# Performance work log

Hardware: AMD Instinct MI355X
Metric: run time of the kernel (lower is better)

Reference implementation:

```python
import jax, jax.numpy as jnp
import numpy as np

B, T, D, H = 2, 2048, 1024, 16
DH = D // H
THETA = 10000.0
MAX_SEQ_LEN = 2048


def setup_inputs() -> dict:
    key = jax.random.key(0)
    kx, kqkv, ko = jax.random.split(key, 3)
    # trunc_normal init matching the torch Linear (std=sqrt(2/(fan_in+fan_out)), clipped at 3 sigma)
    sigma_qkv = (2.0 / (D + 3 * D)) ** 0.5
    sigma_o = (2.0 / (D + D)) ** 0.5
    W_qkv = jax.random.truncated_normal(kqkv, -3.0, 3.0, (3 * D, D), jnp.float32) * sigma_qkv
    W_o = jax.random.truncated_normal(ko, -3.0, 3.0, (D, D), jnp.float32) * sigma_o
    # RoPE caches: angles[t, i] = t / theta^(2i/d_k)
    dims = jnp.arange(0, DH, 2, dtype=jnp.float32)
    inv_freq = 1.0 / (THETA ** (dims / DH))  # [DH/2]
    angles = jnp.arange(MAX_SEQ_LEN, dtype=jnp.float32)[:, None] * inv_freq[None, :]  # [T, DH/2]
    return {
        "x": jax.random.normal(kx, (B, T, D), jnp.float32),
        "token_positions": jnp.arange(T, dtype=jnp.int64 if jax.config.jax_enable_x64 else jnp.int32),
        "W_qkv": W_qkv,
        "W_o": W_o,
        "cos_cached": jnp.cos(angles),
        "sin_cached": jnp.sin(angles),
    }


def _apply_rope(x, cos, sin):
    # x: [b, h, t, dh]; cos/sin: [t, dh/2] broadcast over (b, h)
    x1 = x[..., 0::2]
    x2 = x[..., 1::2]
    r1 = x1 * cos - x2 * sin
    r2 = x1 * sin + x2 * cos
    # interleave back: (.., dh/2, 2) -> (.., dh)
    return jnp.stack([r1, r2], axis=-1).reshape(x.shape)


def reference(x, token_positions, W_qkv, W_o, cos_cached, sin_cached):
    b, t, d = x.shape
    qkv = jnp.einsum("btd,ed->bte", x, W_qkv)  # [b, t, 3d]
    q, k, v = jnp.split(qkv, 3, axis=-1)

    def to_heads(z):
        return z.reshape(b, t, H, DH).transpose(0, 2, 1, 3)  # [b, h, t, dh]

    q, k, v = to_heads(q), to_heads(k), to_heads(v)

    cos = cos_cached[token_positions]  # [t, dh/2]
    sin = sin_cached[token_positions]
    q = _apply_rope(q, cos, sin)
    k = _apply_rope(k, cos, sin)

    scale = 1.0 / jnp.sqrt(jnp.asarray(DH, x.dtype))
    scores = jnp.einsum("bhqd,bhkd->bhqk", q, k) * scale  # full TxT (naive, matches source)
    causal = jnp.tril(jnp.ones((t, t), dtype=bool))  # [t, t]
    scores = jnp.where(causal[None, None, :, :], scores, -jnp.inf)
    attn = jax.nn.softmax(scores, axis=-1)
    out = jnp.einsum("bhqk,bhkd->bhqd", attn, v)  # [b, h, t, dh]
    out = out.transpose(0, 2, 1, 3).reshape(b, t, d)
    return jnp.einsum("btd,ed->bte", out, W_o)
```

## Files before the change

### kernel.cpp

```cpp
#include <hip/hip_runtime.h>
#include <hip/hip_bf16.h>
#include <stdint.h>

#define Bn  2
#define Tn  2048
#define Dn  1024
#define Hn  16
#define DHn 64
#define QSCALE 0.1803368801111204f

typedef unsigned short u16;
typedef __attribute__((ext_vector_type(8))) short s16x8;
typedef __attribute__((ext_vector_type(8))) unsigned short u16x8;
typedef __attribute__((ext_vector_type(4))) unsigned short u16x4;
typedef __attribute__((ext_vector_type(4))) float f32x4;

#define MFMA(a, b, c) __builtin_amdgcn_mfma_f32_16x16x32_bf16((a), (b), (c), 0, 0, 0)

__device__ __forceinline__ u16 f2bf(float f) {
  union { __hip_bfloat16 b; u16 u; } c;
  c.b = __float2bfloat16(f);
  return c.u;
}
__device__ __forceinline__ float bf2f(u16 u) {
  union { u16 u; __hip_bfloat16 b; } c;
  c.u = u;
  return __bfloat162float(c.b);
}

__device__ __forceinline__ void lds16(void* lds, const void* g) {
  __builtin_amdgcn_global_load_lds((__attribute__((address_space(1))) void*)(g),
                                   (__attribute__((address_space(3))) void*)(lds), 16, 0, 0);
}

__global__ __launch_bounds__(256) void k_cvt3(
    const float* __restrict__ s0, int n0,
    const float* __restrict__ s1, int n1,
    const float* __restrict__ s2, int n2,
    u16* __restrict__ d01, u16* __restrict__ d2) {
  int i = blockIdx.x * blockDim.x + threadIdx.x;
  const int stride = gridDim.x * blockDim.x;
  const int nt = n0 + n1 + n2;
  for (; i < nt; i += stride) {
    float4 v;
    u16x4 o;
    if (i < n0 + n1) {
      v = (i < n0) ? ((const float4*)s0)[i] : ((const float4*)s1)[i - n0];
      o[0] = f2bf(v.x); o[1] = f2bf(v.y); o[2] = f2bf(v.z); o[3] = f2bf(v.w);
      ((u16x4*)d01)[i] = o;
    } else {
      v = ((const float4*)s2)[i - n0 - n1];
      o[0] = f2bf(v.x); o[1] = f2bf(v.y); o[2] = f2bf(v.z); o[3] = f2bf(v.w);
      ((u16x4*)d2)[i - n0 - n1] = o;
    }
  }
}

__global__ __launch_bounds__(256) void k_qkv(
    const u16* __restrict__ xb, const u16* __restrict__ wb,
    const int* __restrict__ tokpos,
    const float* __restrict__ cosc, const float* __restrict__ sinc,
    u16* __restrict__ qb, u16* __restrict__ kb, u16* __restrict__ vtb)
{
  __shared__ u16 smem[17408];
  const int tid  = threadIdx.x;
  const int bcol = blockIdx.x;
  const int brow = blockIdx.y;
  const int lane = tid & 63, w = tid >> 6;
  const int wr = w >> 1, wc = w & 1;
  const int l15 = lane & 15, l4 = lane >> 4;
  const int lrow = lane >> 2;
  const int gsw  = (((lane & 3) ^ ((lrow >> 1) & 3)) * 8);
  const int rsw  = (l15 >> 1) & 3;

  const u16* xrow = xb + (size_t)(brow * 128) * 1024;
  const u16* wrow = wb + (size_t)(bcol * 128) * 1024;

  f32x4 acc[4][4] = {};

  {
    const int r0 = w * 32;
    lds16(&smem[r0 * 32],              xrow + (size_t)(r0 + lrow) * 1024 + gsw);
    lds16(&smem[(r0 + 16) * 32],       xrow + (size_t)(r0 + 16 + lrow) * 1024 + gsw);
    lds16(&smem[8192 + r0 * 32],       wrow + (size_t)(r0 + lrow) * 1024 + gsw);
    lds16(&smem[8192 + (r0 + 16) * 32],wrow + (size_t)(r0 + 16 + lrow) * 1024 + gsw);
  }

  for (int kt = 0; kt < 32; ++kt) {
    const int cur = kt & 1;
    const u16* Asb = smem + cur * 4096;
    const u16* Bsb = smem + 8192 + cur * 4096;
    if (kt < 31) {
      u16* Asn = smem + (cur ^ 1) * 4096;
      u16* Bsn = smem + 8192 + (cur ^ 1) * 4096;
      const int k1 = (kt + 1) * 32;
      const int r0 = w * 32;
      lds16(&Asn[r0 * 32],        xrow + (size_t)(r0 + lrow) * 1024 + k1 + gsw);
      lds16(&Asn[(r0 + 16) * 32], xrow + (size_t)(r0 + 16 + lrow) * 1024 + k1 + gsw);
      lds16(&Bsn[r0 * 32],        wrow + (size_t)(r0 + lrow) * 1024 + k1 + gsw);
      lds16(&Bsn[(r0 + 16) * 32], wrow + (size_t)(r0 + 16 + lrow) * 1024 + k1 + gsw);
      asm volatile("s_waitcnt vmcnt(4)" ::: "memory");
    } else {
      asm volatile("s_waitcnt vmcnt(0)" ::: "memory");
    }
    __builtin_amdgcn_s_barrier();
    __builtin_amdgcn_sched_barrier(0);
    __builtin_amdgcn_s_setprio(1);
    {
      const int gr = (l4 ^ rsw) * 8;
      s16x8 af[4], bf[4];
#pragma unroll
      for (int m = 0; m < 4; ++m)
        af[m] = *(const s16x8*)&Asb[(wr * 64 + m * 16 + l15) * 32 + gr];
#pragma unroll
      for (int n = 0; n < 4; ++n)
        bf[n] = *(const s16x8*)&Bsb[(wc * 64 + n * 16 + l15) * 32 + gr];
#pragma unroll
      for (int m = 0; m < 4; ++m)
#pragma unroll
        for (int n = 0; n < 4; ++n)
          acc[m][n] = MFMA(af[m], bf[n], acc[m][n]);
    }
    __builtin_amdgcn_s_setprio(0);
    __builtin_amdgcn_sched_barrier(0);
    __builtin_amdgcn_s_barrier();
  }

#pragma unroll
  for (int m = 0; m < 4; ++m)
#pragma unroll
    for (int n = 0; n < 4; ++n)
#pragma unroll
      for (int r = 0; r < 4; ++r)
        smem[(wr * 64 + m * 16 + l4 * 4 + r) * 136 + wc * 64 + n * 16 + l15] =
            f2bf(acc[m][n][r]);
  __syncthreads();

  if (bcol < 16) {
    u16* dst; float sc;
    if (bcol < 8) { dst = qb; sc = QSCALE; } else { dst = kb; sc = 1.0f; }
#pragma unroll
    for (int ph = 0; ph < 8; ++ph) {
      const int task = ph * 256 + tid;
      const int lr   = task >> 4;
      const int cg   = task & 15;
      const int rowg = brow * 128 + lr;
      const int b = rowg >> 11, t = rowg & 2047;
      const int rem = (bcol * 128 + cg * 8) & 1023;
      const int h = rem >> 6, dh0 = rem & 63;
      u16x8 v = *(const u16x8*)&smem[lr * 136 + cg * 8];
      const int pos = tokpos[t];
      const float4 cv = *(const float4*)&cosc[pos * 32 + (dh0 >> 1)];
      const float4 sv = *(const float4*)&sinc[pos * 32 + (dh0 >> 1)];
      const float cc[4] = {cv.x, cv.y, cv.z, cv.w};
      const float ss[4] = {sv.x, sv.y, sv.z, sv.w};
      u16x8 o;
#pragma unroll
      for (int p = 0; p < 4; ++p) {
        const float x1 = bf2f(v[2 * p]), x2 = bf2f(v[2 * p + 1]);
        o[2 * p]     = f2bf((x1 * cc[p] - x2 * ss[p]) * sc);
        o[2 * p + 1] = f2bf((x1 * ss[p] + x2 * cc[p]) * sc);
      }
      *(u16x8*)(dst + ((size_t)(b * Hn + h) * Tn + t) * DHn + dh0) = o;
    }
  } else {
    const int b  = (brow * 128) >> 11;
    const int t0 = (brow * 128) & 2047;
#pragma unroll
    for (int ph = 0; ph < 8; ++ph) {
      const int task = ph * 256 + tid;
      const int col = task & 127;
      const int tg  = task >> 7;
      const int h  = 2 * (bcol - 16) + (col >> 6);
      const int dh = col & 63;
      u16x8 v;
#pragma unroll
      for (int j = 0; j < 8; ++j) v[j] = smem[(tg * 8 + j) * 136 + col];
      *(u16x8*)(vtb + ((size_t)(b * Hn + h) * DHn + dh) * Tn + t0 + tg * 8) = v;
    }
  }
}

__global__ __launch_bounds__(512) void k_attn(
    const u16* __restrict__ qbuf, const u16* __restrict__ kbuf,
    const u16* __restrict__ vtb, u16* __restrict__ ob)
{
  __shared__ u16 Ks[2][128][64];
  __shared__ u16 Vs[64][128];
  __shared__ u16 Ps[2][8][16][64];

  const int tid  = threadIdx.x;
  const int lane = tid & 63, w = tid >> 6;
  const int l15 = lane & 15, l4 = lane >> 4;
  const int rsw  = l15 & 7;
  const int kgsw = ((lane & 7) ^ (lane >> 3)) * 8;

  const int lin = blockIdx.x;
  const int bh  = lin & 31;
  const int a   = (lin >> 5) & 7, rb = lin >> 8;
  const int qblk = rb ? (15 - a) : a;
  const int b = bh >> 4, h = bh & 15;

  const u16* Qh = qbuf + (size_t)bh * Tn * DHn;
  const u16* Kh = kbuf + (size_t)bh * Tn * DHn;
  const u16* Vh = vtb  + (size_t)bh * DHn * Tn;

  const int q0 = qblk * 128 + w * 16;
  const int ntiles = qblk + 1;

  const s16x8 qf0 = *(const s16x8*)(Qh + (size_t)(q0 + l15) * 64 + l4 * 8);
  const s16x8 qf1 = *(const s16x8*)(Qh + (size_t)(q0 + l15) * 64 + 32 + l4 * 8);

  const s16x8 onesv = {(short)0x3F80, (short)0x3F80, (short)0x3F80, (short)0x3F80,
                       (short)0x3F80, (short)0x3F80, (short)0x3F80, (short)0x3F80};

  f32x4 o[4] = {};
  f32x4 o5 = {};
  float m = -3.0e38f;

  const int vl4 = lane >> 4;

#pragma unroll
  for (int i = 0; i < 2; ++i) {
    const int kr = w * 16 + i * 8;
    lds16(&Ks[0][kr][0], Kh + (size_t)(kr + (lane >> 3)) * 64 + kgsw);
  }

  for (int it = 0; it < ntiles; ++it) {
    const int buf = it & 1;
    const int kv0 = it * 128;
    asm volatile("s_waitcnt vmcnt(0)" ::: "memory");
    __builtin_amdgcn_s_barrier();
    __builtin_amdgcn_sched_barrier(0);

#pragma unroll
    for (int i = 0; i < 2; ++i) {
      const int vr = w * 8 + i * 4;
      const int vrow = vr + vl4;
      lds16(&Vs[vr][0], Vh + (size_t)vrow * Tn + kv0 + ((lane & 15) ^ (vrow & 15)) * 8);
    }
    const bool havek1 = (it + 1 < ntiles);
    if (havek1) {
      const int nb = buf ^ 1;
      const int kv1 = kv0 + 128;
#pragma unroll
      for (int i = 0; i < 2; ++i) {
        const int kr = w * 16 + i * 8;
        lds16(&Ks[nb][kr][0], Kh + (size_t)(kv1 + kr + (lane >> 3)) * 64 + kgsw);
      }
    }

    f32x4 s[8] = {};
    __builtin_amdgcn_s_setprio(1);
#pragma unroll
    for (int ks = 0; ks < 2; ++ks) {
      const s16x8 qf = ks ? qf1 : qf0;
      const int gr = ((ks * 4 + l4) ^ rsw) * 8;
#pragma unroll
      for (int qd = 0; qd < 8; ++qd) {
        const s16x8 kf = *(const s16x8*)&Ks[buf][qd * 16 + l15][gr];
        s[qd] = MFMA(kf, qf, s[qd]);
      }
    }
    __builtin_amdgcn_s_setprio(0);

    if (it == ntiles - 1) {
      const int kvb = kv0 + l4 * 4;
      const int qg  = q0 + l15;
#pragma unroll
      for (int qd = 0; qd < 8; ++qd)
#pragma unroll
        for (int rr = 0; rr < 4; ++rr)
          if (kvb + qd * 16 + rr > qg) s[qd][rr] = -3.0e38f;
    }

    float qm[8];
#pragma unroll
    for (int qd = 0; qd < 8; ++qd)
      qm[qd] = fmaxf(fmaxf(s[qd][0], s[qd][1]), fmaxf(s[qd][2], s[qd][3]));
    float tmax = fmaxf(fmaxf(fmaxf(qm[0], qm[1]), fmaxf(qm[2], qm[3])),
                       fmaxf(fmaxf(qm[4], qm[5]), fmaxf(qm[6], qm[7])));
    tmax = fmaxf(tmax, __shfl_xor(tmax, 16));
    tmax = fmaxf(tmax, __shfl_xor(tmax, 32));

    if (__any(tmax > m + 8.0f)) {
      const float mn    = fmaxf(m, tmax);
      const float alpha = __builtin_amdgcn_exp2f(m - mn);
      m = mn;
#pragma unroll
      for (int n = 0; n < 4; ++n)
#pragma unroll
        for (int rr = 0; rr < 4; ++rr) o[n][rr] *= alpha;
#pragma unroll
      for (int rr = 0; rr < 4; ++rr) o5[rr] *= alpha;
    }

#pragma unroll
    for (int ph = 0; ph < 2; ++ph)
#pragma unroll
      for (int hl = 0; hl < 4; ++hl) {
        const int qd = ph * 4 + hl;
        u16x4 pk;
#pragma unroll
        for (int rr = 0; rr < 4; ++rr)
          pk[rr] = f2bf(__builtin_amdgcn_exp2f(s[qd][rr] - m));
        const int pg = ((hl << 1) + (l4 >> 1)) ^ rsw;
        *(u16x4*)&Ps[ph][w][l15][pg * 8 + (l4 & 1) * 4] = pk;
      }

    if (havek1) asm volatile("s_waitcnt vmcnt(2)" ::: "memory");
    else        asm volatile("s_waitcnt vmcnt(0)" ::: "memory");

    __builtin_amdgcn_s_setprio(1);
#pragma unroll
    for (int ph = 0; ph < 2; ++ph) {
      const s16x8 pf0 = *(const s16x8*)&Ps[ph][w][l15][(l4 ^ rsw) * 8];
      const s16x8 pf1 = *(const s16x8*)&Ps[ph][w][l15][((4 + l4) ^ rsw) * 8];
#pragma unroll
      for (int n = 0; n < 4; ++n) {
        const s16x8 vf0 =
            *(const s16x8*)&Vs[n * 16 + l15][((ph * 8 + l4) ^ l15) * 8];
        const s16x8 vf1 =
            *(const s16x8*)&Vs[n * 16 + l15][((ph * 8 + 4 + l4) ^ l15) * 8];
        o[n] = MFMA(vf0, pf0, o[n]);
        o[n] = MFMA(vf1, pf1, o[n]);
      }
      o5 = MFMA(onesv, pf0, o5);
      o5 = MFMA(onesv, pf1, o5);
    }
    __builtin_amdgcn_s_setprio(0);
    __builtin_amdgcn_sched_barrier(0);
    __builtin_amdgcn_s_barrier();
  }

  const float inv = 1.0f / o5[0];
  const int t = q0 + l15;
#pragma unroll
  for (int n = 0; n < 4; ++n) {
    u16x4 ov;
#pragma unroll
    for (int rr = 0; rr < 4; ++rr) ov[rr] = f2bf(o[n][rr] * inv);
    *(u16x4*)(ob + (size_t)(b * Tn + t) * Dn + h * 64 + n * 16 + l4 * 4) = ov;
  }
}

__global__ __launch_bounds__(256) void k_out(
    const u16* __restrict__ ob, const u16* __restrict__ wob,
    float* __restrict__ out)
{
  __shared__ u16 smem[24576];
  const int tid  = threadIdx.x;
  const int bcol = blockIdx.x;
  const int brow = blockIdx.y;
  const int lane = tid & 63, w = tid >> 6;
  const int wr = w >> 1, wc = w & 1;
  const int l15 = lane & 15, l4 = lane >> 4;
  const int lrow = lane >> 3;
  const int gsw  = ((lane & 7) ^ (lane >> 3)) * 8;
  const int rsw  = l15 & 7;

  f32x4 acc[4][2] = {};

#pragma unroll
  for (int c = 0; c < 4; ++c) {
    const int r0 = w * 32 + c * 8;
    lds16(&smem[r0 * 64], ob + (size_t)(brow * 128 + r0 + lrow) * 1024 + gsw);
  }
#pragma unroll
  for (int c = 0; c < 2; ++c) {
    const int r0 = w * 16 + c * 8;
    lds16(&smem[16384 + r0 * 64], wob + (size_t)(bcol * 64 + r0 + lrow) * 1024 + gsw);
  }

  for (int kt = 0; kt < 16; ++kt) {
    const int cur = kt & 1;
    const u16* Asb = smem + cur * 8192;
    const u16* Bsb = smem + 16384 + cur * 4096;
    if (kt < 15) {
      u16* Asn = smem + (cur ^ 1) * 8192;
      u16* Bsn = smem + 16384 + (cur ^ 1) * 4096;
      const int k1 = (kt + 1) * 64;
#pragma unroll
      for (int c = 0; c < 4; ++c) {
        const int r0 = w * 32 + c * 8;
        lds16(&Asn[r0 * 64], ob + (size_t)(brow * 128 + r0 + lrow) * 1024 + k1 + gsw);
      }
#pragma unroll
      for (int c = 0; c < 2; ++c) {
        const int r0 = w * 16 + c * 8;
        lds16(&Bsn[r0 * 64], wob + (size_t)(bcol * 64 + r0 + lrow) * 1024 + k1 + gsw);
      }
      asm volatile("s_waitcnt vmcnt(6)" ::: "memory");
    } else {
      asm volatile("s_waitcnt vmcnt(0)" ::: "memory");
    }
    __builtin_amdgcn_s_barrier();
    __builtin_amdgcn_sched_barrier(0);
    __builtin_amdgcn_s_setprio(1);
#pragma unroll
    for (int kk = 0; kk < 64; kk += 32) {
      const int gc = (kk >> 3) + l4;
      s16x8 af[4], bf[2];
#pragma unroll
      for (int m = 0; m < 4; ++m)
        af[m] = *(const s16x8*)&Asb[(wr * 64 + m * 16 + l15) * 64 + ((gc ^ rsw) * 8)];
#pragma unroll
      for (int n = 0; n < 2; ++n)
        bf[n] = *(const s16x8*)&Bsb[(wc * 32 + n * 16 + l15) * 64 + ((gc ^ rsw) * 8)];
#pragma unroll
      for (int m = 0; m < 4; ++m)
#pragma unroll
        for (int n = 0; n < 2; ++n)
          acc[m][n] = MFMA(af[m], bf[n], acc[m][n]);
    }
    __builtin_amdgcn_s_setprio(0);
    __builtin_amdgcn_sched_barrier(0);
    __builtin_amdgcn_s_barrier();
  }

#pragma unroll
  for (int m = 0; m < 4; ++m) {
    const int rowb = brow * 128 + wr * 64 + m * 16 + l4 * 4;
#pragma unroll
    for (int n = 0; n < 2; ++n) {
      const int colg = bcol * 64 + wc * 32 + n * 16 + l15;
#pragma unroll
      for (int r = 0; r < 4; ++r)
        out[(size_t)(rowb + r) * 1024 + colg] = acc[m][n][r];
    }
  }
}

extern "C" void kernel_launch(void* const* d_in, const int* in_sizes, int n_in,
                              void* d_out, int out_size, void* d_ws, size_t ws_size,
                              hipStream_t stream) {
  const float* x      = (const float*)d_in[0];
  const int*   tokpos = (const int*)d_in[1];
  const float* wqkv   = (const float*)d_in[2];
  const float* wo     = (const float*)d_in[3];
  const float* cosc   = (const float*)d_in[4];
  const float* sinc   = (const float*)d_in[5];
  float* out = (float*)d_out;

  u16* xb    = (u16*)d_ws;
  u16* wqkvb = xb + (size_t)Bn * Tn * Dn;
  u16* qb    = wqkvb + (size_t)3 * Dn * Dn;
  u16* kb    = qb + (size_t)Bn * Tn * Dn;
  u16* vtb   = kb + (size_t)Bn * Tn * Dn;
  u16* wob   = vtb + (size_t)Bn * Tn * Dn;
  u16* ob    = xb;

  dim3 blk(256);
  k_cvt3<<<dim3(2048), blk, 0, stream>>>(x, (Bn * Tn * Dn) / 4,
                                         wqkv, (3 * Dn * Dn) / 4,
                                         wo, (Dn * Dn) / 4, xb, wob);

  k_qkv<<<dim3(24, 32), blk, 0, stream>>>(xb, wqkvb, tokpos, cosc, sinc, qb, kb, vtb);

  k_attn<<<dim3(512), dim3(512), 0, stream>>>(qb, kb, vtb, ob);

  k_out<<<dim3(16, 32), blk, 0, stream>>>(ob, wob, out);
}
```

Measured before the change: 99.89 us.

## Drop K double buffering and single-buffer P to shrink attention LDS footprint

Removes the double-buffered K tile and the two-phase P staging buffer in the attention kernel. K and V are now loaded at the start of each iteration behind extra barriers, and the second half of P is written into the same buffer between PV phases. This roughly halves shared memory per block, presumably to fit more blocks per CU, but it drops the overlap of the next K load with compute and adds barriers. The reuse of the P buffer within a wave also looks racy without a wave-level sync between phases.

```diff
diff --git a/kernel.cpp b/kernel.cpp
--- a/kernel.cpp
+++ b/kernel.cpp
@@ -185,9 +185,9 @@
     const u16* __restrict__ qbuf, const u16* __restrict__ kbuf,
     const u16* __restrict__ vtb, u16* __restrict__ ob)
 {
-  __shared__ u16 Ks[2][128][64];
+  __shared__ u16 Ks[128][64];
   __shared__ u16 Vs[64][128];
-  __shared__ u16 Ps[2][8][16][64];
+  __shared__ u16 Ps[8][16][64];
 
   const int tid  = threadIdx.x;
   const int lane = tid & 63, w = tid >> 6;
@@ -220,35 +220,26 @@
 
   const int vl4 = lane >> 4;
 
-#pragma unroll
-  for (int i = 0; i < 2; ++i) {
-    const int kr = w * 16 + i * 8;
-    lds16(&Ks[0][kr][0], Kh + (size_t)(kr + (lane >> 3)) * 64 + kgsw);
-  }
-
   for (int it = 0; it < ntiles; ++it) {
-    const int buf = it & 1;
     const int kv0 = it * 128;
-    asm volatile("s_waitcnt vmcnt(0)" ::: "memory");
-    __builtin_amdgcn_s_barrier();
-    __builtin_amdgcn_sched_barrier(0);
-
+
+    __builtin_amdgcn_s_barrier();
+    __builtin_amdgcn_sched_barrier(0);
+
+#pragma unroll
+    for (int i = 0; i < 2; ++i) {
+      const int kr = w * 16 + i * 8;
+      lds16(&Ks[kr][0], Kh + (size_t)(kv0 + kr + (lane >> 3)) * 64 + kgsw);
+    }
 #pragma unroll
     for (int i = 0; i < 2; ++i) {
       const int vr = w * 8 + i * 4;
       const int vrow = vr + vl4;
       lds16(&Vs[vr][0], Vh + (size_t)vrow * Tn + kv0 + ((lane & 15) ^ (vrow & 15)) * 8);
     }
-    const bool havek1 = (it + 1 < ntiles);
-    if (havek1) {
-      const int nb = buf ^ 1;
-      const int kv1 = kv0 + 128;
-#pragma unroll
-      for (int i = 0; i < 2; ++i) {
-        const int kr = w * 16 + i * 8;
-        lds16(&Ks[nb][kr][0], Kh + (size_t)(kv1 + kr + (lane >> 3)) * 64 + kgsw);
-      }
-    }
+    asm volatile("s_waitcnt vmcnt(2)" ::: "memory");
+    __builtin_amdgcn_s_barrier();
+    __builtin_amdgcn_sched_barrier(0);
 
     f32x4 s[8] = {};
     __builtin_amdgcn_s_setprio(1);
@@ -258,7 +249,7 @@
       const int gr = ((ks * 4 + l4) ^ rsw) * 8;
 #pragma unroll
       for (int qd = 0; qd < 8; ++qd) {
-        const s16x8 kf = *(const s16x8*)&Ks[buf][qd * 16 + l15][gr];
+        const s16x8 kf = *(const s16x8*)&Ks[qd * 16 + l15][gr];
         s[qd] = MFMA(kf, qf, s[qd]);
       }
     }
@@ -296,26 +287,36 @@
     }
 
 #pragma unroll
-    for (int ph = 0; ph < 2; ++ph)
-#pragma unroll
-      for (int hl = 0; hl < 4; ++hl) {
-        const int qd = ph * 4 + hl;
-        u16x4 pk;
-#pragma unroll
-        for (int rr = 0; rr < 4; ++rr)
-          pk[rr] = f2bf(__builtin_amdgcn_exp2f(s[qd][rr] - m));
-        const int pg = ((hl << 1) + (l4 >> 1)) ^ rsw;
-        *(u16x4*)&Ps[ph][w][l15][pg * 8 + (l4 & 1) * 4] = pk;
-      }
-
-    if (havek1) asm volatile("s_waitcnt vmcnt(2)" ::: "memory");
-    else        asm volatile("s_waitcnt vmcnt(0)" ::: "memory");
+    for (int hl = 0; hl < 4; ++hl) {
+      u16x4 pk;
+#pragma unroll
+      for (int rr = 0; rr < 4; ++rr)
+        pk[rr] = f2bf(__builtin_amdgcn_exp2f(s[hl][rr] - m));
+      const int pg = ((hl << 1) + (l4 >> 1)) ^ rsw;
+      *(u16x4*)&Ps[w][l15][pg * 8 + (l4 & 1) * 4] = pk;
+    }
+
+    asm volatile("s_waitcnt vmcnt(0)" ::: "memory");
+    __builtin_amdgcn_s_barrier();
+    __builtin_amdgcn_sched_barrier(0);
 
     __builtin_amdgcn_s_setprio(1);
 #pragma unroll
     for (int ph = 0; ph < 2; ++ph) {
-      const s16x8 pf0 = *(const s16x8*)&Ps[ph][w][l15][(l4 ^ rsw) * 8];
-      const s16x8 pf1 = *(const s16x8*)&Ps[ph][w][l15][((4 + l4) ^ rsw) * 8];
+      if (ph == 1) {
+#pragma unroll
+        for (int hl = 0; hl < 4; ++hl) {
+          const int qd = 4 + hl;
+          u16x4 pk;
+#pragma unroll
+          for (int rr = 0; rr < 4; ++rr)
+            pk[rr] = f2bf(__builtin_amdgcn_exp2f(s[qd][rr] - m));
+          const int pg = ((hl << 1) + (l4 >> 1)) ^ rsw;
+          *(u16x4*)&Ps[w][l15][pg * 8 + (l4 & 1) * 4] = pk;
+        }
+      }
+      const s16x8 pf0 = *(const s16x8*)&Ps[w][l15][(l4 ^ rsw) * 8];
+      const s16x8 pf1 = *(const s16x8*)&Ps[w][l15][((4 + l4) ^ rsw) * 8];
 #pragma unroll
       for (int n = 0; n < 4; ++n) {
         const s16x8 vf0 =
@@ -330,7 +331,6 @@
     }
     __builtin_amdgcn_s_setprio(0);
     __builtin_amdgcn_sched_barrier(0);
-    __builtin_amdgcn_s_barrier();
   }
 
   const float inv = 1.0f / o5[0];
```

Result: faster. 97.64 us (median of 2 runs) (-2.3%).
